# Kernel tuning notes

Measured on AMD Instinct MI355X. Metric: run time of the kernel, lower is better.

The kernel has to match this reference:

```python
import jax, jax.numpy as jnp
import numpy as np

B, D, H, O = 4096, 1024, 8192, 1000

def setup_inputs() -> dict:
    key = jax.random.key(0)
    k1, k2, k3 = jax.random.split(key, 3)
    x = jax.random.normal(k1, (B, D), dtype=jnp.float32)
    kohonen_weights = jax.random.normal(k2, (H, D), dtype=jnp.float32) * (6.0 / (H + D)) ** 0.5
    grossberg_weights = jax.random.normal(k3, (O, H), dtype=jnp.float32) * (6.0 / (O + H)) ** 0.5
    return {"x": x, "kohonen_weights": kohonen_weights, "grossberg_weights": grossberg_weights}

def reference(x, kohonen_weights, grossberg_weights):
    # but kept faithful since distances only feed argmin -> same winners either way)
    x_sq = jnp.sum(x * x, axis=1, keepdims=True)                      # [B,1]
    w_sq = jnp.sum(kohonen_weights * kohonen_weights, axis=1)         # [H]
    sq_dists = x_sq - 2.0 * (x @ kohonen_weights.T) + w_sq[None, :]   # [B,H]
    winners = jnp.argmin(sq_dists, axis=1)                            # [B]
    # one_hot @ grossberg.T is mathematically a row gather of grossberg.T
    output = grossberg_weights.T[winners]                             # [B,O]
    return output, winners
```

## Files before the change

kernel.cpp:

```cpp
#include <hip/hip_runtime.h>
#include <hip/hip_bf16.h>

#define B_ 4096
#define D_ 1024
#define H_ 8192
#define O_ 1000

#define BM 128
#define BN 128
#define BK 64

typedef __attribute__((ext_vector_type(8))) short short8;
typedef __attribute__((ext_vector_type(4))) short short4v;
typedef __attribute__((ext_vector_type(4))) float f32x4;

union BF4 { __hip_bfloat16 b[4]; short4v s; };

__global__ __launch_bounds__(256) void split_rows_kernel(
    const float* __restrict__ src,
    __hip_bfloat16* __restrict__ hi,
    __hip_bfloat16* __restrict__ lo,
    float* __restrict__ sq)
{
  const int row = blockIdx.x;
  const int t = threadIdx.x;
  const float4 v = ((const float4*)(src + (size_t)row * D_))[t];

  float ss = v.x * v.x + v.y * v.y + v.z * v.z + v.w * v.w;

  BF4 Hh, Ll;
  const float e[4] = {v.x, v.y, v.z, v.w};
#pragma unroll
  for (int i = 0; i < 4; ++i) {
    __hip_bfloat16 h = __float2bfloat16(e[i]);
    float r = e[i] - __bfloat162float(h);
    Hh.b[i] = h;
    Ll.b[i] = __float2bfloat16(r);
  }
  const int kb = t >> 4;
  const int u = ((t >> 1) & 7) ^ (row & 7);
  const int dst = kb * 64 + u * 8 + (t & 1) * 4;
  *(short4v*)(hi + (size_t)row * D_ + dst) = Hh.s;
  *(short4v*)(lo + (size_t)row * D_ + dst) = Ll.s;

#pragma unroll
  for (int off = 32; off > 0; off >>= 1) ss += __shfl_down(ss, off);
  __shared__ float wsum[4];
  if ((t & 63) == 0) wsum[t >> 6] = ss;
  __syncthreads();
  if (t == 0) sq[row] = (wsum[0] + wsum[1]) + (wsum[2] + wsum[3]);
}

__device__ __forceinline__ void gload16(void* lds, const void* g) {
  __builtin_amdgcn_global_load_lds(
      (const __attribute__((address_space(1))) unsigned int*)g,
      (__attribute__((address_space(3))) unsigned int*)lds, 16, 0, 0);
}

#define MFMA_BF16 __builtin_amdgcn_mfma_f32_16x16x32_bf16

__global__ __launch_bounds__(256, 2) void gemm_argmin_kernel(
    const __hip_bfloat16* __restrict__ xh, const __hip_bfloat16* __restrict__ xl,
    const __hip_bfloat16* __restrict__ wh, const __hip_bfloat16* __restrict__ wl,
    const float* __restrict__ xsq, const float* __restrict__ wsq,
    unsigned long long* __restrict__ keys)
{
  __shared__ __hip_bfloat16 sAh[BM * BK], sAl[BM * BK];
  __shared__ __hip_bfloat16 sBh[BN * BK], sBl[BN * BK];

  const int t = threadIdx.x;
  const int brow = blockIdx.y * BM;
  const int bcol = blockIdx.x * BN;

  const int lane = t & 63;
  const int wid = t >> 6;
  const int wr = (wid >> 1) * 64;
  const int wc = (wid & 1) * 64;

  const int trow = t >> 3;
  const int tu8 = (t & 7) * 8;

  const __hip_bfloat16* gAh = xh + (size_t)(brow + trow) * D_ + tu8;
  const __hip_bfloat16* gAl = xl + (size_t)(brow + trow) * D_ + tu8;
  const __hip_bfloat16* gBh = wh + (size_t)(bcol + trow) * D_ + tu8;
  const __hip_bfloat16* gBl = wl + (size_t)(bcol + trow) * D_ + tu8;

  f32x4 acc[4][4] = {};

  const int cc = lane & 15;
  const int q = lane >> 4;
  const int swz = lane & 7;

  for (int kt = 0; kt < D_ / BK; ++kt) {
    const int ko = kt * BK;
#pragma unroll
    for (int p = 0; p < 4; ++p) {
      const size_t go = (size_t)p * 32 * D_ + ko;
      gload16(sAh + t * 8 + p * 2048, gAh + go);
      gload16(sAl + t * 8 + p * 2048, gAl + go);
      gload16(sBh + t * 8 + p * 2048, gBh + go);
      gload16(sBl + t * 8 + p * 2048, gBl + go);
    }
    __syncthreads();

#pragma unroll
    for (int kk = 0; kk < 2; ++kk) {
      short8 ah[4], al[4], bh[4], bl[4];
      const int uu = ((kk * 4 + q) ^ swz) * 8;
#pragma unroll
      for (int m = 0; m < 4; ++m) {
        const int off = (wr + m * 16 + cc) * BK + uu;
        ah[m] = *(const short8*)(sAh + off);
        al[m] = *(const short8*)(sAl + off);
      }
#pragma unroll
      for (int n = 0; n < 4; ++n) {
        const int off = (wc + n * 16 + cc) * BK + uu;
        bh[n] = *(const short8*)(sBh + off);
        bl[n] = *(const short8*)(sBl + off);
      }
#pragma unroll
      for (int m = 0; m < 4; ++m)
#pragma unroll
        for (int n = 0; n < 4; ++n) {
          acc[m][n] = MFMA_BF16(ah[m], bh[n], acc[m][n], 0, 0, 0);
          acc[m][n] = MFMA_BF16(al[m], bh[n], acc[m][n], 0, 0, 0);
          acc[m][n] = MFMA_BF16(ah[m], bl[n], acc[m][n], 0, 0, 0);
        }
    }
    __syncthreads();
  }

#pragma unroll
  for (int m = 0; m < 4; ++m) {
#pragma unroll
    for (int r = 0; r < 4; ++r) {
      const int row = brow + wr + m * 16 + q * 4 + r;
      const float xs = xsq[row];
      unsigned long long best = ~0ULL;
#pragma unroll
      for (int n = 0; n < 4; ++n) {
        const int col = bcol + wc + n * 16 + cc;
        const float s = (xs - 2.0f * acc[m][n][r]) + wsq[col];
        unsigned ub = __float_as_uint(s);
        ub = (ub & 0x80000000u) ? ~ub : (ub | 0x80000000u);
        const unsigned long long key =
            ((unsigned long long)ub << 32) | (unsigned)col;
        if (key < best) best = key;
      }
#pragma unroll
      for (int off2 = 1; off2 < 16; off2 <<= 1) {
        const unsigned long long o = __shfl_xor(best, off2);
        if (o < best) best = o;
      }
      if (cc == 0) atomicMin(&keys[row], best);
    }
  }
}

__global__ __launch_bounds__(256) void transposeG_kernel(
    const float* __restrict__ G, float* __restrict__ GT)
{
  __shared__ float tile[32][33];
  const int h0 = blockIdx.x * 32;
  const int o0 = blockIdx.y * 32;
  const int tx = threadIdx.x;
  const int ty = threadIdx.y;
#pragma unroll
  for (int j = 0; j < 4; ++j) {
    const int o = o0 + ty + j * 8;
    if (o < O_) tile[ty + j * 8][tx] = G[(size_t)o * H_ + h0 + tx];
  }
  __syncthreads();
  const int o = o0 + tx;
  if (o < O_) {
#pragma unroll
    for (int j = 0; j < 4; ++j) {
      GT[(size_t)(h0 + ty + j * 8) * O_ + o] = tile[tx][ty + j * 8];
    }
  }
}

__global__ __launch_bounds__(256) void finalize_kernel(
    const unsigned long long* __restrict__ keys,
    const float* __restrict__ GT, float* __restrict__ out)
{
  const int b = blockIdx.x;
  const unsigned w = (unsigned)(keys[b] & 0xFFFFFFFFull);
  if (threadIdx.x == 0) out[(size_t)B_ * O_ + b] = (float)w;
  const float4* src = (const float4*)(GT + (size_t)w * O_);
  float4* dst = (float4*)(out + (size_t)b * O_);
  for (int i = threadIdx.x; i < O_ / 4; i += 256) dst[i] = src[i];
}

extern "C" void kernel_launch(void* const* d_in, const int* in_sizes, int n_in,
                              void* d_out, int out_size, void* d_ws, size_t ws_size,
                              hipStream_t stream)
{
  (void)in_sizes; (void)n_in; (void)out_size; (void)ws_size;
  const float* x = (const float*)d_in[0];
  const float* kw = (const float*)d_in[1];
  const float* gw = (const float*)d_in[2];
  float* out = (float*)d_out;

  char* ws = (char*)d_ws;
  __hip_bfloat16* xh = (__hip_bfloat16*)(ws);
  __hip_bfloat16* xl = (__hip_bfloat16*)(ws + 8388608);
  __hip_bfloat16* wh = (__hip_bfloat16*)(ws + 16777216);
  __hip_bfloat16* wl = (__hip_bfloat16*)(ws + 33554432);
  float* xsq = (float*)(ws + 50331648);
  float* wsq = (float*)(ws + 50331648 + 16384);
  unsigned long long* keys = (unsigned long long*)(ws + 50331648 + 16384 + 32768);
  float* GT = (float*)(ws + 16777216);

  hipMemsetAsync(keys, 0xFF, B_ * sizeof(unsigned long long), stream);
  split_rows_kernel<<<B_, 256, 0, stream>>>(x, xh, xl, xsq);
  split_rows_kernel<<<H_, 256, 0, stream>>>(kw, wh, wl, wsq);
  gemm_argmin_kernel<<<dim3(H_ / BN, B_ / BM), 256, 0, stream>>>(
      xh, xl, wh, wl, xsq, wsq, keys);
  transposeG_kernel<<<dim3(H_ / 32, (O_ + 31) / 32), dim3(32, 8), 0, stream>>>(gw, GT);
  finalize_kernel<<<B_, 256, 0, stream>>>(keys, GT, out);
}
```

Measured before the change: 253.2 us.

## Restructure split-bf16 GEMM-argmin into 256x256 tiles with a 4-stage LDS pipeline

The GEMM-argmin kernel moves to 256x256 block tiles with 512 threads and 32x32x16 bf16 MFMAs. The hi/lo operands are packed into one K=2048 row with a new swizzle. The three split products run as 96 K=32 steps through a 4-deep asynchronous global-to-LDS pipeline, using explicit vmcnt waits, a single barrier per step and raised wave priority around the MFMAs. The aim is more data reuse per load and overlap of memory traffic with matrix math. In exchange it uses 128KB of LDS, which limits occupancy to one block per CU, and it relies on hand-counted outstanding-load waits.

After: 313.3 us. +23.8%, slower.

```diff
diff --git a/kernel.cpp b/kernel.cpp
--- a/kernel.cpp
+++ b/kernel.cpp
@@ -5,27 +5,28 @@
 #define D_ 1024
 #define H_ 8192
 #define O_ 1000
-
-#define BM 128
-#define BN 128
-#define BK 64
+#define K2 2048
+#define NSTEP 96
 
 typedef __attribute__((ext_vector_type(8))) short short8;
 typedef __attribute__((ext_vector_type(4))) short short4v;
-typedef __attribute__((ext_vector_type(4))) float f32x4;
+typedef __attribute__((ext_vector_type(16))) float f32x16;
 
 union BF4 { __hip_bfloat16 b[4]; short4v s; };
 
+__device__ __forceinline__ void gload16(void* ldsp, const void* g) {
+  __builtin_amdgcn_global_load_lds(
+      (const __attribute__((address_space(1))) unsigned int*)g,
+      (__attribute__((address_space(3))) unsigned int*)ldsp, 16, 0, 0);
+}
+
 __global__ __launch_bounds__(256) void split_rows_kernel(
-    const float* __restrict__ src,
-    __hip_bfloat16* __restrict__ hi,
-    __hip_bfloat16* __restrict__ lo,
+    const float* __restrict__ src, __hip_bfloat16* __restrict__ dst,
     float* __restrict__ sq)
 {
-  const int row = blockIdx.x;
+  const int r = blockIdx.x;
   const int t = threadIdx.x;
-  const float4 v = ((const float4*)(src + (size_t)row * D_))[t];
-
+  const float4 v = ((const float4*)(src + (size_t)r * D_))[t];
   float ss = v.x * v.x + v.y * v.y + v.z * v.z + v.w * v.w;
 
   BF4 Hh, Ll;
@@ -33,115 +34,113 @@
 #pragma unroll
   for (int i = 0; i < 4; ++i) {
     __hip_bfloat16 h = __float2bfloat16(e[i]);
-    float r = e[i] - __bfloat162float(h);
     Hh.b[i] = h;
-    Ll.b[i] = __float2bfloat16(r);
-  }
-  const int kb = t >> 4;
-  const int u = ((t >> 1) & 7) ^ (row & 7);
-  const int dst = kb * 64 + u * 8 + (t & 1) * 4;
-  *(short4v*)(hi + (size_t)row * D_ + dst) = Hh.s;
-  *(short4v*)(lo + (size_t)row * D_ + dst) = Ll.s;
-
-#pragma unroll
-  for (int off = 32; off > 0; off >>= 1) ss += __shfl_down(ss, off);
+    Ll.b[i] = __float2bfloat16(e[i] - __bfloat162float(h));
+  }
+  const int c = t >> 3;
+  const int u = (t >> 1) & 3;
+  const int up = u ^ ((r >> 1) & 3);
+  const int off = c * 32 + up * 8 + (t & 1) * 4;
+  __hip_bfloat16* base = dst + (size_t)r * K2;
+  *(short4v*)(base + off) = Hh.s;
+  *(short4v*)(base + 1024 + off) = Ll.s;
+
+#pragma unroll
+  for (int o = 32; o > 0; o >>= 1) ss += __shfl_down(ss, o);
   __shared__ float wsum[4];
   if ((t & 63) == 0) wsum[t >> 6] = ss;
   __syncthreads();
-  if (t == 0) sq[row] = (wsum[0] + wsum[1]) + (wsum[2] + wsum[3]);
-}
-
-__device__ __forceinline__ void gload16(void* lds, const void* g) {
-  __builtin_amdgcn_global_load_lds(
-      (const __attribute__((address_space(1))) unsigned int*)g,
-      (__attribute__((address_space(3))) unsigned int*)lds, 16, 0, 0);
-}
-
-#define MFMA_BF16 __builtin_amdgcn_mfma_f32_16x16x32_bf16
-
-__global__ __launch_bounds__(256, 2) void gemm_argmin_kernel(
-    const __hip_bfloat16* __restrict__ xh, const __hip_bfloat16* __restrict__ xl,
-    const __hip_bfloat16* __restrict__ wh, const __hip_bfloat16* __restrict__ wl,
+  if (t == 0) sq[r] = (wsum[0] + wsum[1]) + (wsum[2] + wsum[3]);
+}
+
+__global__ __launch_bounds__(512, 2) void gemm_argmin_kernel(
+    const __hip_bfloat16* __restrict__ Ap, const __hip_bfloat16* __restrict__ Bp,
     const float* __restrict__ xsq, const float* __restrict__ wsq,
     unsigned long long* __restrict__ keys)
 {
-  __shared__ __hip_bfloat16 sAh[BM * BK], sAl[BM * BK];
-  __shared__ __hip_bfloat16 sBh[BN * BK], sBl[BN * BK];
+  __shared__ char lds[131072];
 
   const int t = threadIdx.x;
-  const int brow = blockIdx.y * BM;
-  const int bcol = blockIdx.x * BN;
-
+  const int brow = blockIdx.y * 256;
+  const int bcol = blockIdx.x * 256;
   const int lane = t & 63;
   const int wid = t >> 6;
-  const int wr = (wid >> 1) * 64;
-  const int wc = (wid & 1) * 64;
-
-  const int trow = t >> 3;
-  const int tu8 = (t & 7) * 8;
-
-  const __hip_bfloat16* gAh = xh + (size_t)(brow + trow) * D_ + tu8;
-  const __hip_bfloat16* gAl = xl + (size_t)(brow + trow) * D_ + tu8;
-  const __hip_bfloat16* gBh = wh + (size_t)(bcol + trow) * D_ + tu8;
-  const __hip_bfloat16* gBl = wl + (size_t)(bcol + trow) * D_ + tu8;
-
-  f32x4 acc[4][4] = {};
-
-  const int cc = lane & 15;
-  const int q = lane >> 4;
-  const int swz = lane & 7;
-
-  for (int kt = 0; kt < D_ / BK; ++kt) {
-    const int ko = kt * BK;
-#pragma unroll
-    for (int p = 0; p < 4; ++p) {
-      const size_t go = (size_t)p * 32 * D_ + ko;
-      gload16(sAh + t * 8 + p * 2048, gAh + go);
-      gload16(sAl + t * 8 + p * 2048, gAl + go);
-      gload16(sBh + t * 8 + p * 2048, gBh + go);
-      gload16(sBl + t * 8 + p * 2048, gBl + go);
+  const int wm = wid >> 2;
+  const int wn = wid & 3;
+  const int c31 = lane & 31;
+  const int q = lane >> 5;
+  const int xr = (c31 >> 1) & 3;
+  const int up0 = ((0 * 2 + q) ^ xr) * 16;
+  const int up1 = ((1 * 2 + q) ^ xr) * 16;
+
+  const int g0 = t, g1 = t + 512;
+  const __hip_bfloat16* gA0 = Ap + (size_t)(brow + (g0 >> 2)) * K2 + (g0 & 3) * 8;
+  const __hip_bfloat16* gA1 = Ap + (size_t)(brow + (g1 >> 2)) * K2 + (g1 & 3) * 8;
+  const __hip_bfloat16* gB0 = Bp + (size_t)(bcol + (g0 >> 2)) * K2 + (g0 & 3) * 8;
+  const __hip_bfloat16* gB1 = Bp + (size_t)(bcol + (g1 >> 2)) * K2 + (g1 & 3) * 8;
+
+  const int abase = (wm * 128 + c31) * 64;
+  const int bbase = 16384 + (wn * 64 + c31) * 64;
+
+  auto STAGE = [&](int j) {
+    char* buf = lds + (j & 3) * 32768;
+    const int ao = (((j >> 5) == 1) ? 1024 : 0) + (j & 31) * 32;
+    const int bo = (((j >> 5) == 2) ? 1024 : 0) + (j & 31) * 32;
+    gload16(buf + g0 * 16, gA0 + ao);
+    gload16(buf + g1 * 16, gA1 + ao);
+    gload16(buf + 16384 + g0 * 16, gB0 + bo);
+    gload16(buf + 16384 + g1 * 16, gB1 + bo);
+  };
+
+  f32x16 acc[4][2] = {};
+
+  STAGE(0); STAGE(1); STAGE(2);
+
+  for (int j = 0; j < NSTEP; ++j) {
+    if (j < NSTEP - 2)       asm volatile("s_waitcnt vmcnt(8)" ::: "memory");
+    else if (j == NSTEP - 2) asm volatile("s_waitcnt vmcnt(4)" ::: "memory");
+    else                     asm volatile("s_waitcnt vmcnt(0)" ::: "memory");
+    __builtin_amdgcn_s_barrier();
+
+    const char* buf = lds + (j & 3) * 32768;
+    short8 af[4][2], bf[2][2];
+#pragma unroll
+    for (int fm = 0; fm < 4; ++fm) {
+      af[fm][0] = *(const short8*)(buf + abase + fm * 2048 + up0);
+      af[fm][1] = *(const short8*)(buf + abase + fm * 2048 + up1);
     }
-    __syncthreads();
-
-#pragma unroll
-    for (int kk = 0; kk < 2; ++kk) {
-      short8 ah[4], al[4], bh[4], bl[4];
-      const int uu = ((kk * 4 + q) ^ swz) * 8;
-#pragma unroll
-      for (int m = 0; m < 4; ++m) {
-        const int off = (wr + m * 16 + cc) * BK + uu;
-        ah[m] = *(const short8*)(sAh + off);
-        al[m] = *(const short8*)(sAl + off);
+#pragma unroll
+    for (int fn = 0; fn < 2; ++fn) {
+      bf[fn][0] = *(const short8*)(buf + bbase + fn * 2048 + up0);
+      bf[fn][1] = *(const short8*)(buf + bbase + fn * 2048 + up1);
+    }
+
+    if (j + 3 < NSTEP) STAGE(j + 3);
+
+    __builtin_amdgcn_s_setprio(1);
+#pragma unroll
+    for (int fm = 0; fm < 4; ++fm)
+#pragma unroll
+      for (int fn = 0; fn < 2; ++fn) {
+        acc[fm][fn] = __builtin_amdgcn_mfma_f32_32x32x16_bf16(
+            af[fm][0], bf[fn][0], acc[fm][fn], 0, 0, 0);
+        acc[fm][fn] = __builtin_amdgcn_mfma_f32_32x32x16_bf16(
+            af[fm][1], bf[fn][1], acc[fm][fn], 0, 0, 0);
       }
-#pragma unroll
-      for (int n = 0; n < 4; ++n) {
-        const int off = (wc + n * 16 + cc) * BK + uu;
-        bh[n] = *(const short8*)(sBh + off);
-        bl[n] = *(const short8*)(sBl + off);
-      }
-#pragma unroll
-      for (int m = 0; m < 4; ++m)
-#pragma unroll
-        for (int n = 0; n < 4; ++n) {
-          acc[m][n] = MFMA_BF16(ah[m], bh[n], acc[m][n], 0, 0, 0);
-          acc[m][n] = MFMA_BF16(al[m], bh[n], acc[m][n], 0, 0, 0);
-          acc[m][n] = MFMA_BF16(ah[m], bl[n], acc[m][n], 0, 0, 0);
-        }
-    }
-    __syncthreads();
-  }
-
-#pragma unroll
-  for (int m = 0; m < 4; ++m) {
-#pragma unroll
-    for (int r = 0; r < 4; ++r) {
-      const int row = brow + wr + m * 16 + q * 4 + r;
+    __builtin_amdgcn_s_setprio(0);
+  }
+
+#pragma unroll
+  for (int fm = 0; fm < 4; ++fm) {
+#pragma unroll
+    for (int rg = 0; rg < 16; ++rg) {
+      const int row = brow + wm * 128 + fm * 32 + (rg & 3) + 8 * (rg >> 2) + 4 * q;
       const float xs = xsq[row];
       unsigned long long best = ~0ULL;
 #pragma unroll
-      for (int n = 0; n < 4; ++n) {
-        const int col = bcol + wc + n * 16 + cc;
-        const float s = (xs - 2.0f * acc[m][n][r]) + wsq[col];
+      for (int fn = 0; fn < 2; ++fn) {
+        const int col = bcol + wn * 64 + fn * 32 + c31;
+        const float s = (xs - 2.0f * acc[fm][fn][rg]) + wsq[col];
         unsigned ub = __float_as_uint(s);
         ub = (ub & 0x80000000u) ? ~ub : (ub | 0x80000000u);
         const unsigned long long key =
@@ -149,11 +148,11 @@
         if (key < best) best = key;
       }
 #pragma unroll
-      for (int off2 = 1; off2 < 16; off2 <<= 1) {
-        const unsigned long long o = __shfl_xor(best, off2);
-        if (o < best) best = o;
+      for (int o = 1; o <= 16; o <<= 1) {
+        const unsigned long long v = __shfl_xor(best, o);
+        if (v < best) best = v;
       }
-      if (cc == 0) atomicMin(&keys[row], best);
+      if (c31 == 0) atomicMin(&keys[row], best);
     }
   }
 }
@@ -175,9 +174,8 @@
   const int o = o0 + tx;
   if (o < O_) {
 #pragma unroll
-    for (int j = 0; j < 4; ++j) {
+    for (int j = 0; j < 4; ++j)
       GT[(size_t)(h0 + ty + j * 8) * O_ + o] = tile[tx][ty + j * 8];
-    }
   }
 }
 
@@ -204,20 +202,18 @@
   float* out = (float*)d_out;
 
   char* ws = (char*)d_ws;
-  __hip_bfloat16* xh = (__hip_bfloat16*)(ws);
-  __hip_bfloat16* xl = (__hip_bfloat16*)(ws + 8388608);
-  __hip_bfloat16* wh = (__hip_bfloat16*)(ws + 16777216);
-  __hip_bfloat16* wl = (__hip_bfloat16*)(ws + 33554432);
+  __hip_bfloat16* Ap = (__hip_bfloat16*)(ws);
+  __hip_bfloat16* Bp = (__hip_bfloat16*)(ws + 16777216);
   float* xsq = (float*)(ws + 50331648);
   float* wsq = (float*)(ws + 50331648 + 16384);
   unsigned long long* keys = (unsigned long long*)(ws + 50331648 + 16384 + 32768);
-  float* GT = (float*)(ws + 16777216);
+  float* GT = (float*)(ws);
 
   hipMemsetAsync(keys, 0xFF, B_ * sizeof(unsigned long long), stream);
-  split_rows_kernel<<<B_, 256, 0, stream>>>(x, xh, xl, xsq);
-  split_rows_kernel<<<H_, 256, 0, stream>>>(kw, wh, wl, wsq);
-  gemm_argmin_kernel<<<dim3(H_ / BN, B_ / BM), 256, 0, stream>>>(
-      xh, xl, wh, wl, xsq, wsq, keys);
+  split_rows_kernel<<<B_, 256, 0, stream>>>(x, Ap, xsq);
+  split_rows_kernel<<<H_, 256, 0, stream>>>(kw, Bp, wsq);
+  gemm_argmin_kernel<<<dim3(H_ / 256, B_ / 256), 512, 0, stream>>>(
+      Ap, Bp, xsq, wsq, keys);
   transposeG_kernel<<<dim3(H_ / 32, (O_ + 31) / 32), dim3(32, 8), 0, stream>>>(gw, GT);
   finalize_kernel<<<B_, 256, 0, stream>>>(keys, GT, out);
 }
```
